# Kernel optimization log

Hardware: AMD Instinct MI355X
Metric: run time of the kernel (lower is better)

The kernel has to match this reference:

```python
import jax, jax.numpy as jnp
import numpy as np


def setup_inputs() -> dict:
    key = jax.random.key(0)
    k1, k2 = jax.random.split(key)
    B, C, H, W = 4, 256, 128, 128
    x1 = jax.random.normal(k1, (B, C, H, W), dtype=jnp.float32)
    x2 = jax.random.normal(k2, (B, C, H, W), dtype=jnp.float32)
    return {"x1": x1, "x2": x2, "d": 4}


def reference(x1, x2, d):
    # Windowed correlation cost volume: for each offset (i,j) in a
    # (2d+1)x(2d+1) window, mean over channels of x1 * shifted(x2).
    B, C, H, W = x1.shape
    out_dim = 2 * d + 1
    x2p = jnp.pad(x2, ((0, 0), (0, 0), (d, d), (d, d)))  # [B,C,H+2d,W+2d]
    inv_c = jnp.asarray(1.0 / C, dtype=x1.dtype)
    # Fixed small loop over 81 structural offsets; each term fuses
    # multiply + channel-sum.
    cv = [
        jnp.sum(x1 * jax.lax.dynamic_slice(x2p, (0, 0, i, j), (B, C, H, W)), axis=1) * inv_c
        for i in range(out_dim)
        for j in range(out_dim)
    ]
    return jnp.stack(cv, axis=1)  # [B, (2d+1)^2, H, W]
```

## Files before the change

kernel.cpp:

```cpp
#include <hip/hip_runtime.h>

namespace {

constexpr int Cn   = 256;
constexpr int Hh   = 128;
constexpr int Ww   = 128;
constexpr int HW   = Hh * Ww;
constexpr int TILE = 16;
constexpr int CCH  = 8;
constexpr int NCH  = Cn / CCH;
constexpr int HALO = 4;
constexpr int X2T  = 24;
constexpr int X2S  = 48;
constexpr int X2CH = X2T * X2S;
constexpr int NOFF = 81;


__global__ __launch_bounds__(576, 1)
void costvol_kernel(const float* __restrict__ x1,
                    const float* __restrict__ x2,
                    float* __restrict__ out)
{
  __shared__ float s2[2][CCH * X2CH];

  const int t    = threadIdx.x;
  const int wv   = t >> 6;
  const int lane = t & 63;
  const int h    = lane >> 2;
  const int m    = lane & 3;

  const int tx = blockIdx.x, ty = blockIdx.y, b = blockIdx.z;
  const int x0 = tx * TILE, y0 = ty * TILE;

  const float* g1 = x1 + (size_t)b * Cn * HW + (size_t)(y0 + h) * Ww + (x0 + 4 * m);
  const float* g2 = x2 + (size_t)b * Cn * HW;

  const int   g    = t / 72;
  const int   r    = t % 72;
  const int   rrow = r / 24;
  const int   rcol = r % 24;
  const float* gc  = g2 + (size_t)g * HW;

  const int  gx   = x0 - HALO + rcol;
  const bool gxok = ((unsigned)gx < (unsigned)Ww);
  int  off[8];
  bool val[8];
#pragma unroll
  for (int j = 0; j < 8; ++j) {
    const int gy = y0 - HALO + rrow + 3 * j;
    const bool ok = gxok && ((unsigned)gy < (unsigned)Hh);
    val[j] = ok;
    off[j] = ok ? (gy * Ww + gx) : 0;
  }
  const int lbase = g * X2CH + rrow * X2S + rcol;

  float rs[8];
  auto stage_load = [&](int k) {
    const size_t cb = (size_t)(k * CCH) * HW;
#pragma unroll
    for (int j = 0; j < 8; ++j)
      rs[j] = val[j] ? gc[cb + off[j]] : 0.0f;
  };
  auto stage_write = [&](int nb) {
    float* s = s2[nb];
#pragma unroll
    for (int j = 0; j < 8; ++j)
      s[lbase + j * 3 * X2S] = rs[j];
  };

  float acc[9][4];
#pragma unroll
  for (int d = 0; d < 9; ++d)
#pragma unroll
    for (int p = 0; p < 4; ++p) acc[d][p] = 0.0f;

  const int rbase = (h + wv) * X2S + 4 * m;

  auto half = [&](int k, int hc, const float* sc) {
    float4 a[4];
    float  w[4][12];
#pragma unroll
    for (int cc = 0; cc < 4; ++cc) {
      a[cc] = *reinterpret_cast<const float4*>(
          g1 + (size_t)(k * CCH + 4 * hc + cc) * HW);
      const float* bp = sc + (4 * hc + cc) * X2CH + rbase;
      *reinterpret_cast<float4*>(w[cc])     = *reinterpret_cast<const float4*>(bp);
      *reinterpret_cast<float4*>(w[cc] + 4) = *reinterpret_cast<const float4*>(bp + 4);
      *reinterpret_cast<float4*>(w[cc] + 8) = *reinterpret_cast<const float4*>(bp + 8);
    }
#pragma unroll
    for (int cc = 0; cc < 4; ++cc)
#pragma unroll
      for (int dj = 0; dj < 9; ++dj) {
        acc[dj][0] = fmaf(a[cc].x, w[cc][dj + 0], acc[dj][0]);
        acc[dj][1] = fmaf(a[cc].y, w[cc][dj + 1], acc[dj][1]);
        acc[dj][2] = fmaf(a[cc].z, w[cc][dj + 2], acc[dj][2]);
        acc[dj][3] = fmaf(a[cc].w, w[cc][dj + 3], acc[dj][3]);
      }
  };

  stage_load(0);
  stage_write(0);
  __syncthreads();

  for (int k = 0; k < NCH; ++k) {
    if (k + 1 < NCH) stage_load(k + 1);
    const float* sc = s2[k & 1];
    half(k, 0, sc);
    if (k + 1 < NCH) stage_write((k + 1) & 1);
    half(k, 1, sc);
    __syncthreads();
  }

  const float invc = 1.0f / (float)Cn;
  const int y  = y0 + h;
  const int xb = x0 + 4 * m;
#pragma unroll
  for (int dj = 0; dj < 9; ++dj) {
    const int o = wv * 9 + dj;
    float4 v;
    v.x = acc[dj][0] * invc;
    v.y = acc[dj][1] * invc;
    v.z = acc[dj][2] * invc;
    v.w = acc[dj][3] * invc;
    *reinterpret_cast<float4*>(out + (((size_t)b * NOFF + o) * Hh + y) * Ww + xb) = v;
  }
}

}

extern "C" void kernel_launch(void* const* d_in, const int* in_sizes, int n_in,
                              void* d_out, int out_size, void* d_ws, size_t ws_size,
                              hipStream_t stream) {
  const float* x1 = (const float*)d_in[0];
  const float* x2 = (const float*)d_in[1];
  float* out = (float*)d_out;

  dim3 grid(Ww / TILE, Hh / TILE, 4);
  dim3 block(576);
  costvol_kernel<<<grid, block, 0, stream>>>(x1, x2, out);
}
```

Baseline: 75.38 us.

## Vectorize x2 halo staging to float4 and prefetch two chunks ahead

The x2 halo tile is now staged with float4 global loads and float4 LDS stores, two per thread, where it was eight scalar loads per thread. The staging pipeline now holds two register buffers, so each chunk's global load is issued two iterations before it is consumed. This is meant to cut load instruction count and hide global latency better. It adds register pressure under a 576-thread launch bound, and it leaves a dead, odd-looking 'ok' expression in place.

```diff
diff --git a/kernel.cpp b/kernel.cpp
--- a/kernel.cpp
+++ b/kernel.cpp
@@ -13,6 +13,8 @@
 constexpr int X2T  = 24;
 constexpr int X2S  = 48;
 constexpr int X2CH = X2T * X2S;
+constexpr int SC4  = 6;
+constexpr int NF4  = CCH * X2T * SC4;
 constexpr int NOFF = 81;
 
 
@@ -35,37 +37,37 @@
   const float* g1 = x1 + (size_t)b * Cn * HW + (size_t)(y0 + h) * Ww + (x0 + 4 * m);
   const float* g2 = x2 + (size_t)b * Cn * HW;
 
-  const int   g    = t / 72;
-  const int   r    = t % 72;
-  const int   rrow = r / 24;
-  const int   rcol = r % 24;
-  const float* gc  = g2 + (size_t)g * HW;
+  int  soff[2], swr[2];
+  bool sval[2];
+#pragma unroll
+  for (int j = 0; j < 2; ++j) {
+    const int f    = t + 576 * j;
+    const int ch   = f / (X2T * SC4);
+    const int rem  = f % (X2T * SC4);
+    const int row  = rem / SC4, col4 = rem % SC4;
+    const int gy = y0 - HALO + row;
+    const int gx = x0 - HALO + 4 * col4;
+    const bool ok = ((unsigned)gy < (unsigned)Hh) &&
+                    (gx >= 0) && (gx + 3 < Ww + 1 + 3) && (gx + 3 <= Ww - 1 + 0 + 3) &&
+                    (gx + 3 <= 127 + 3) && (gx <= Ww - 4 + 3) && (gx + 3 < Ww + 4) && (gx < Ww) && (gx >= 0);
+    sval[j] = ((unsigned)gy < (unsigned)Hh) && (gx >= 0) && (gx + 3 < Ww);
+    soff[j] = sval[j] ? (ch * HW + gy * Ww + gx) : 0;
+    swr[j]  = ch * X2CH + row * X2S + 4 * col4;
+  }
 
-  const int  gx   = x0 - HALO + rcol;
-  const bool gxok = ((unsigned)gx < (unsigned)Ww);
-  int  off[8];
-  bool val[8];
-#pragma unroll
-  for (int j = 0; j < 8; ++j) {
-    const int gy = y0 - HALO + rrow + 3 * j;
-    const bool ok = gxok && ((unsigned)gy < (unsigned)Hh);
-    val[j] = ok;
-    off[j] = ok ? (gy * Ww + gx) : 0;
-  }
-  const int lbase = g * X2CH + rrow * X2S + rcol;
-
-  float rs[8];
-  auto stage_load = [&](int k) {
+  float4 rs[2][2];
+  auto stage_load = [&](int k, int pr) {
     const size_t cb = (size_t)(k * CCH) * HW;
 #pragma unroll
-    for (int j = 0; j < 8; ++j)
-      rs[j] = val[j] ? gc[cb + off[j]] : 0.0f;
+    for (int j = 0; j < 2; ++j)
+      rs[pr][j] = sval[j] ? *reinterpret_cast<const float4*>(g2 + cb + soff[j])
+                          : float4{0.f, 0.f, 0.f, 0.f};
   };
-  auto stage_write = [&](int nb) {
+  auto stage_write = [&](int nb, int pr) {
     float* s = s2[nb];
 #pragma unroll
-    for (int j = 0; j < 8; ++j)
-      s[lbase + j * 3 * X2S] = rs[j];
+    for (int j = 0; j < 2; ++j)
+      *reinterpret_cast<float4*>(s + swr[j]) = rs[pr][j];
   };
 
   float acc[9][4];
@@ -99,15 +101,17 @@
       }
   };
 
-  stage_load(0);
-  stage_write(0);
+  stage_load(0, 0);
+  stage_write(0, 0);
+  stage_load(1, 1);
   __syncthreads();
 
   for (int k = 0; k < NCH; ++k) {
-    if (k + 1 < NCH) stage_load(k + 1);
+    const int pn = (k + 1) & 1;
+    if (k + 1 < NCH) stage_write(pn, pn);
+    if (k + 2 < NCH) stage_load(k + 2, k & 1);
     const float* sc = s2[k & 1];
     half(k, 0, sc);
-    if (k + 1 < NCH) stage_write((k + 1) & 1);
     half(k, 1, sc);
     __syncthreads();
   }
```

Result: slower. 108.0 us (+43.3%).

## Stage x2 halo tiles via direct global-to-LDS 16-byte loads

Applied to the files above, without the earlier changes.

Replaces the register-staged x2 tile loads (global load into registers, then LDS write) with buffer global_load_lds 16-byte transfers straight into shared memory. The LDS row stride shrinks from 48 to 24 floats, and each thread issues two float4 copies per channel chunk. Out-of-bounds threads read from a zeroed workspace buffer that is set with a memset before launch. This removes the LDS write instructions and frees registers. The cost is an added memset call and a full vmcnt wait before each barrier, and the 24-float stride may cause LDS bank conflicts on reads.

```diff
diff --git a/kernel.cpp b/kernel.cpp
--- a/kernel.cpp
+++ b/kernel.cpp
@@ -11,14 +11,21 @@
 constexpr int NCH  = Cn / CCH;
 constexpr int HALO = 4;
 constexpr int X2T  = 24;
-constexpr int X2S  = 48;
+constexpr int X2S  = 24;
 constexpr int X2CH = X2T * X2S;
 constexpr int NOFF = 81;
 
 
+__device__ __forceinline__ void gl2lds16(const float* g, float* l) {
+  __builtin_amdgcn_global_load_lds(
+      (const __attribute__((address_space(1))) void*)g,
+      (__attribute__((address_space(3))) void*)l, 16, 0, 0);
+}
+
 __global__ __launch_bounds__(576, 1)
 void costvol_kernel(const float* __restrict__ x1,
                     const float* __restrict__ x2,
+                    const float* __restrict__ zp,
                     float* __restrict__ out)
 {
   __shared__ float s2[2][CCH * X2CH];
@@ -35,38 +42,25 @@
   const float* g1 = x1 + (size_t)b * Cn * HW + (size_t)(y0 + h) * Ww + (x0 + 4 * m);
   const float* g2 = x2 + (size_t)b * Cn * HW;
 
-  const int   g    = t / 72;
-  const int   r    = t % 72;
-  const int   rrow = r / 24;
-  const int   rcol = r % 24;
-  const float* gc  = g2 + (size_t)g * HW;
+  const float* gp0;  size_t inc0;
+  const float* gp1;  size_t inc1;
+  {
+    const int s = t, ch = s / 144, rem = s % 144, row = rem / 6, c4 = rem % 6;
+    const int gy = y0 - HALO + row, gx = x0 - HALO + 4 * c4;
+    const bool ok = ((unsigned)gy < (unsigned)Hh) && (gx >= 0) && (gx + 3 < Ww);
+    gp0  = ok ? (g2 + (size_t)ch * HW + (size_t)gy * Ww + gx) : zp;
+    inc0 = ok ? (size_t)(CCH * HW) : 0;
+  }
+  {
+    const int s = t + 576, ch = s / 144, rem = s % 144, row = rem / 6, c4 = rem % 6;
+    const int gy = y0 - HALO + row, gx = x0 - HALO + 4 * c4;
+    const bool ok = ((unsigned)gy < (unsigned)Hh) && (gx >= 0) && (gx + 3 < Ww);
+    gp1  = ok ? (g2 + (size_t)ch * HW + (size_t)gy * Ww + gx) : zp;
+    inc1 = ok ? (size_t)(CCH * HW) : 0;
+  }
 
-  const int  gx   = x0 - HALO + rcol;
-  const bool gxok = ((unsigned)gx < (unsigned)Ww);
-  int  off[8];
-  bool val[8];
-#pragma unroll
-  for (int j = 0; j < 8; ++j) {
-    const int gy = y0 - HALO + rrow + 3 * j;
-    const bool ok = gxok && ((unsigned)gy < (unsigned)Hh);
-    val[j] = ok;
-    off[j] = ok ? (gy * Ww + gx) : 0;
-  }
-  const int lbase = g * X2CH + rrow * X2S + rcol;
-
-  float rs[8];
-  auto stage_load = [&](int k) {
-    const size_t cb = (size_t)(k * CCH) * HW;
-#pragma unroll
-    for (int j = 0; j < 8; ++j)
-      rs[j] = val[j] ? gc[cb + off[j]] : 0.0f;
-  };
-  auto stage_write = [&](int nb) {
-    float* s = s2[nb];
-#pragma unroll
-    for (int j = 0; j < 8; ++j)
-      s[lbase + j * 3 * X2S] = rs[j];
-  };
+  const int lds0 = (t >> 6) * 256;
+  const int lds1 = lds0 + 9 * 256;
 
   float acc[9][4];
 #pragma unroll
@@ -76,7 +70,7 @@
 
   const int rbase = (h + wv) * X2S + 4 * m;
 
-  auto half = [&](int k, int hc, const float* sc) {
+  auto quad = [&](int k, int hc, const float* sc) {
     float4 a[4];
     float  w[4][12];
 #pragma unroll
@@ -99,16 +93,21 @@
       }
   };
 
-  stage_load(0);
-  stage_write(0);
+  gl2lds16(gp0, &s2[0][lds0]);  gp0 += inc0;
+  gl2lds16(gp1, &s2[0][lds1]);  gp1 += inc1;
+  asm volatile("s_waitcnt vmcnt(0)" ::: "memory");
   __syncthreads();
 
   for (int k = 0; k < NCH; ++k) {
-    if (k + 1 < NCH) stage_load(k + 1);
+    if (k + 1 < NCH) {
+      float* nb = s2[(k + 1) & 1];
+      gl2lds16(gp0, nb + lds0);  gp0 += inc0;
+      gl2lds16(gp1, nb + lds1);  gp1 += inc1;
+    }
     const float* sc = s2[k & 1];
-    half(k, 0, sc);
-    if (k + 1 < NCH) stage_write((k + 1) & 1);
-    half(k, 1, sc);
+    quad(k, 0, sc);
+    quad(k, 1, sc);
+    asm volatile("s_waitcnt vmcnt(0)" ::: "memory");
     __syncthreads();
   }
 
@@ -136,7 +135,9 @@
   const float* x2 = (const float*)d_in[1];
   float* out = (float*)d_out;
 
+  hipMemsetAsync(d_ws, 0, 256, stream);
+
   dim3 grid(Ww / TILE, Hh / TILE, 4);
   dim3 block(576);
-  costvol_kernel<<<grid, block, 0, stream>>>(x1, x2, out);
+  costvol_kernel<<<grid, block, 0, stream>>>(x1, x2, (const float*)d_ws, out);
 }
```

Result: slower. 79.49 us (+5.5%).
